# Kernel tuning notes

Hardware: AMD Instinct MI355X
Metric: run time of the kernel (lower is better)

The kernel has to match this reference:

```python
import jax, jax.numpy as jnp
import numpy as np

N = 1_048_576      # flattened batch (forward reshapes to (-1, 4))
Q_DIM = 4
HIDDEN = 64
DC = Q_DIM // 2    # q_dim_changed = 2
NUM_LO = (DC * DC - DC) // 2  # = 1
SLOPE = 0.01       # torch leaky_relu default negative slope


def setup_inputs() -> dict:
    key = jax.random.key(0)
    ks = jax.random.split(key, 9)
    def lin(kw, kb, fan_out, fan_in):
        bound = 1.0 / np.sqrt(fan_in)
        W = jax.random.uniform(kw, (fan_out, fan_in), jnp.float32, -bound, bound)
        b = jax.random.uniform(kb, (fan_out,), jnp.float32, -bound, bound)
        return W, b
    x = jax.random.normal(ks[0], (N, Q_DIM), jnp.float32)
    W1, b1 = lin(ks[1], ks[2], HIDDEN, Q_DIM)
    W2, b2 = lin(ks[3], ks[4], HIDDEN, HIDDEN)
    W_Ld, b_Ld = lin(ks[5], ks[6], DC, HIDDEN)
    W_Lo, b_Lo = lin(ks[7], ks[8], NUM_LO, HIDDEN)
    return {"x": x, "W1": W1, "b1": b1, "W2": W2, "b2": b2,
            "W_Ld": W_Ld, "b_Ld": b_Ld, "W_Lo": W_Lo, "b_Lo": b_Lo}


def reference(x, W1, b1, W2, b2, W_Ld, b_Ld, W_Lo, b_Lo):
    q = x.reshape(-1, Q_DIM)                      # (n, 4)
    n = q.shape[0]
    h1 = jax.nn.leaky_relu(q @ W1.T + b1, SLOPE)  # (n, 64)
    h2 = jax.nn.leaky_relu(h1 @ W2.T + b2, SLOPE) # (n, 64); dropout is eval-mode identity
    Ld = jax.nn.softplus(h2 @ W_Ld.T + b_Ld)      # (n, 2) positive diagonal
    Lo = h2 @ W_Lo.T + b_Lo                       # (n, 1) strictly-lower entries
    rows, cols = jnp.tril_indices(DC, -1)         # strictly lower triangle, row-major
    diag = jnp.arange(DC)
    L = jnp.zeros((n, DC, DC), dtype=q.dtype)
    L = L.at[:, rows, cols].set(Lo)               # scatter Lo (matches torch boolean-mask fill order)
    L = L.at[:, diag, diag].set(Ld)               # diag_embed(Ld)
    H = jnp.einsum('nij,nkj->nik', L, L) + 1e-9 * jnp.eye(DC, dtype=q.dtype)
    return H
```

## Files before the change

kernel.cpp:

```cpp
#include <hip/hip_runtime.h>


typedef __attribute__((ext_vector_type(8))) short bf16x8;
typedef __attribute__((ext_vector_type(4))) float f32x4;

#define ROWS_PER_BLOCK 256

__device__ __forceinline__ float lrelu(float a) {
    return fmaxf(a, 0.01f * a);
}

__device__ __forceinline__ float softplus(float v) {
    return fmaxf(v, 0.0f) + log1pf(expf(-fabsf(v)));
}

__device__ __forceinline__ unsigned cvt_pk_bf16(float lo, float hi) {
    unsigned r;
    asm("v_cvt_pk_bf16_f32 %0, %1, %2" : "=v"(r) : "v"(lo), "v"(hi));
    return r;
}

__global__ __launch_bounds__(256, 3) void dln_mfma(
    const float* __restrict__ x,
    const float* __restrict__ W1,  const float* __restrict__ b1,
    const float* __restrict__ W2,  const float* __restrict__ b2,
    const float* __restrict__ WLd, const float* __restrict__ bLd,
    const float* __restrict__ WLo, const float* __restrict__ bLo,
    float* __restrict__ out)
{
    __shared__ __align__(16) unsigned short h1s[4][8][64][8];

    const int tid  = threadIdx.x;
    const int lane = tid & 63;
    const int wv   = tid >> 6;
    const int quad = lane >> 4;
    const int c    = lane & 15;

    bf16x8 afrag[4][2];
    f32x4 wld0[4], wld1[4], wlo[4], b2v[4];
#pragma unroll
    for (int mt = 0; mt < 4; ++mt) {
        const float* wr = W2 + (16 * mt + c) * 64 + 8 * quad;
#pragma unroll
        for (int s = 0; s < 2; ++s) {
            const float4 f0 = *(const float4*)(wr + 32 * s);
            const float4 f1 = *(const float4*)(wr + 32 * s + 4);
            uint4 u;
            u.x = cvt_pk_bf16(f0.x, f0.y);
            u.y = cvt_pk_bf16(f0.z, f0.w);
            u.z = cvt_pk_bf16(f1.x, f1.y);
            u.w = cvt_pk_bf16(f1.z, f1.w);
            afrag[mt][s] = __builtin_bit_cast(bf16x8, u);
        }
        const int nb = 16 * mt + 4 * quad;
        wld0[mt] = *(const f32x4*)(WLd + nb);
        wld1[mt] = *(const f32x4*)(WLd + 64 + nb);
        wlo[mt]  = *(const f32x4*)(WLo + nb);
        b2v[mt]  = *(const f32x4*)(b2 + nb);
    }

    const int row_g = blockIdx.x * ROWS_PER_BLOCK + tid;
    {
        const float4 qv = ((const float4*)x)[row_g];
#pragma unroll
        for (int ch = 0; ch < 8; ++ch) {
            unsigned up[4];
#pragma unroll
            for (int p = 0; p < 4; ++p) {
                float h[2];
#pragma unroll
                for (int e = 0; e < 2; ++e) {
                    const int j = ch * 8 + p * 2 + e;
                    float a = b1[j];
                    a = fmaf(qv.x, W1[4 * j + 0], a);
                    a = fmaf(qv.y, W1[4 * j + 1], a);
                    a = fmaf(qv.z, W1[4 * j + 2], a);
                    a = fmaf(qv.w, W1[4 * j + 3], a);
                    h[e] = lrelu(a);
                }
                up[p] = cvt_pk_bf16(h[0], h[1]);
            }
            *(uint4*)&h1s[wv][ch][lane][0] = make_uint4(up[0], up[1], up[2], up[3]);
        }
    }

    float sld0 = 0.0f, sld1 = 0.0f, slo = 0.0f;
#pragma unroll
    for (int it = 0; it < 4; ++it) {
        const bf16x8 b0 = *(const bf16x8*)&h1s[wv][quad][it * 16 + c][0];
        const bf16x8 b1f = *(const bf16x8*)&h1s[wv][4 + quad][it * 16 + c][0];

        float pld0 = 0.0f, pld1 = 0.0f, plo = 0.0f;
#pragma unroll
        for (int mt = 0; mt < 4; ++mt) {
            f32x4 acc = b2v[mt];
            acc = __builtin_amdgcn_mfma_f32_16x16x32_bf16(afrag[mt][0], b0, acc, 0, 0, 0);
            acc = __builtin_amdgcn_mfma_f32_16x16x32_bf16(afrag[mt][1], b1f, acc, 0, 0, 0);
#pragma unroll
            for (int r = 0; r < 4; ++r) {
                const float h2 = lrelu(acc[r]);
                pld0 = fmaf(h2, wld0[mt][r], pld0);
                pld1 = fmaf(h2, wld1[mt][r], pld1);
                plo  = fmaf(h2, wlo[mt][r],  plo);
            }
        }
        pld0 += __shfl_xor(pld0, 16); pld0 += __shfl_xor(pld0, 32);
        pld1 += __shfl_xor(pld1, 16); pld1 += __shfl_xor(pld1, 32);
        plo  += __shfl_xor(plo,  16); plo  += __shfl_xor(plo,  32);
        if (it == quad) { sld0 = pld0; sld1 = pld1; slo = plo; }
    }

    {
        const float ld0 = softplus(sld0 + bLd[0]);
        const float ld1 = softplus(sld1 + bLd[1]);
        const float lo  = slo + bLo[0];
        float4 o;
        o.x = fmaf(ld0, ld0, 1e-9f);
        o.y = ld0 * lo;
        o.z = o.y;
        o.w = fmaf(lo, lo, fmaf(ld1, ld1, 1e-9f));
        reinterpret_cast<float4*>(out)[row_g] = o;
    }
}

__global__ __launch_bounds__(256) void dln_tail(
    const float* __restrict__ x,
    const float* __restrict__ W1,  const float* __restrict__ b1,
    const float* __restrict__ W2,  const float* __restrict__ b2,
    const float* __restrict__ WLd, const float* __restrict__ bLd,
    const float* __restrict__ WLo, const float* __restrict__ bLo,
    float* __restrict__ out, int row0, int nrows)
{
    const int row = row0 + blockIdx.x * 256 + threadIdx.x;
    if (row >= nrows) return;
    const float4 qv = reinterpret_cast<const float4*>(x)[row];
    float h1[64];
#pragma unroll
    for (int j = 0; j < 64; ++j) {
        float a = b1[j];
        a = fmaf(qv.x, W1[4 * j + 0], a);
        a = fmaf(qv.y, W1[4 * j + 1], a);
        a = fmaf(qv.z, W1[4 * j + 2], a);
        a = fmaf(qv.w, W1[4 * j + 3], a);
        h1[j] = lrelu(a);
    }
    float ld0 = bLd[0], ld1 = bLd[1], lo = bLo[0];
#pragma unroll 4
    for (int j = 0; j < 64; ++j) {
        float a0 = b2[j], a1 = 0.0f;
        const float* w = W2 + 64 * j;
#pragma unroll
        for (int k = 0; k < 64; k += 2) {
            a0 = fmaf(h1[k],     w[k],     a0);
            a1 = fmaf(h1[k + 1], w[k + 1], a1);
        }
        const float a = lrelu(a0 + a1);
        ld0 = fmaf(a, WLd[j],      ld0);
        ld1 = fmaf(a, WLd[64 + j], ld1);
        lo  = fmaf(a, WLo[j],      lo);
    }
    ld0 = softplus(ld0);
    ld1 = softplus(ld1);
    float4 o;
    o.x = fmaf(ld0, ld0, 1e-9f);
    o.y = ld0 * lo;
    o.z = o.y;
    o.w = fmaf(lo, lo, fmaf(ld1, ld1, 1e-9f));
    reinterpret_cast<float4*>(out)[row] = o;
}

extern "C" void kernel_launch(void* const* d_in, const int* in_sizes, int n_in,
                              void* d_out, int out_size, void* d_ws, size_t ws_size,
                              hipStream_t stream)
{
    const float* x   = (const float*)d_in[0];
    const float* W1  = (const float*)d_in[1];
    const float* b1  = (const float*)d_in[2];
    const float* W2  = (const float*)d_in[3];
    const float* b2  = (const float*)d_in[4];
    const float* WLd = (const float*)d_in[5];
    const float* bLd = (const float*)d_in[6];
    const float* WLo = (const float*)d_in[7];
    const float* bLo = (const float*)d_in[8];
    float* out = (float*)d_out;

    const int nrows = in_sizes[0] / 4;
    const int nfull = nrows / ROWS_PER_BLOCK;
    const int rem   = nrows - nfull * ROWS_PER_BLOCK;

    if (nfull > 0)
        dln_mfma<<<nfull, 256, 0, stream>>>(
            x, W1, b1, W2, b2, WLd, bLd, WLo, bLo, out);
    if (rem > 0)
        dln_tail<<<(rem + 255) / 256, 256, 0, stream>>>(
            x, W1, b1, W2, b2, WLd, bLd, WLo, bLo, out,
            nfull * ROWS_PER_BLOCK, nrows);
}
```

Measured before the change: 129.4 us.

## Process four 256-row groups per block to amortize weight fragment loads

Each block now handles 1024 rows by looping four times over 256-row groups. The W2 bf16 fragments and the head weights are loaded and converted once per block rather than once per 256 rows. All four x rows are prefetched up front, and the launch-bounds occupancy hint rises from 3 to 4. The trade-off is a quarter as many blocks, longer per-block serial work, and possibly more register pressure from the prefetched inputs. The intra-wave LDS reuse across iterations needs no barrier because each wave owns its own slice.

Result: slower. 164.1 us (+26.8%).

```diff
diff --git a/kernel.cpp b/kernel.cpp
--- a/kernel.cpp
+++ b/kernel.cpp
@@ -4,7 +4,8 @@
 typedef __attribute__((ext_vector_type(8))) short bf16x8;
 typedef __attribute__((ext_vector_type(4))) float f32x4;
 
-#define ROWS_PER_BLOCK 256
+#define ROWS_PER_BLOCK 1024
+#define G_ITERS 4
 
 __device__ __forceinline__ float lrelu(float a) {
     return fmaxf(a, 0.01f * a);
@@ -20,7 +21,7 @@
     return r;
 }
 
-__global__ __launch_bounds__(256, 3) void dln_mfma(
+__global__ __launch_bounds__(256, 4) void dln_mfma(
     const float* __restrict__ x,
     const float* __restrict__ W1,  const float* __restrict__ b1,
     const float* __restrict__ W2,  const float* __restrict__ b2,
@@ -35,6 +36,12 @@
     const int wv   = tid >> 6;
     const int quad = lane >> 4;
     const int c    = lane & 15;
+
+    const int row0 = blockIdx.x * ROWS_PER_BLOCK + tid;
+    const float4 qv0 = ((const float4*)x)[row0];
+    const float4 qv1 = ((const float4*)x)[row0 + 256];
+    const float4 qv2 = ((const float4*)x)[row0 + 512];
+    const float4 qv3 = ((const float4*)x)[row0 + 768];
 
     bf16x8 afrag[4][2];
     f32x4 wld0[4], wld1[4], wlo[4], b2v[4];
@@ -58,10 +65,15 @@
         wlo[mt]  = *(const f32x4*)(WLo + nb);
         b2v[mt]  = *(const f32x4*)(b2 + nb);
     }
-
-    const int row_g = blockIdx.x * ROWS_PER_BLOCK + tid;
-    {
-        const float4 qv = ((const float4*)x)[row_g];
+    const float bld0 = bLd[0];
+    const float bld1 = bLd[1];
+    const float blo0 = bLo[0];
+
+#pragma unroll
+    for (int g = 0; g < G_ITERS; ++g) {
+        const float4 qv = (g == 0) ? qv0 : (g == 1) ? qv1 : (g == 2) ? qv2 : qv3;
+        const int row_g = row0 + g * 256;
+
 #pragma unroll
         for (int ch = 0; ch < 8; ++ch) {
             unsigned up[4];
@@ -82,44 +94,44 @@
             }
             *(uint4*)&h1s[wv][ch][lane][0] = make_uint4(up[0], up[1], up[2], up[3]);
         }
-    }
-
-    float sld0 = 0.0f, sld1 = 0.0f, slo = 0.0f;
-#pragma unroll
-    for (int it = 0; it < 4; ++it) {
-        const bf16x8 b0 = *(const bf16x8*)&h1s[wv][quad][it * 16 + c][0];
-        const bf16x8 b1f = *(const bf16x8*)&h1s[wv][4 + quad][it * 16 + c][0];
-
-        float pld0 = 0.0f, pld1 = 0.0f, plo = 0.0f;
-#pragma unroll
-        for (int mt = 0; mt < 4; ++mt) {
-            f32x4 acc = b2v[mt];
-            acc = __builtin_amdgcn_mfma_f32_16x16x32_bf16(afrag[mt][0], b0, acc, 0, 0, 0);
-            acc = __builtin_amdgcn_mfma_f32_16x16x32_bf16(afrag[mt][1], b1f, acc, 0, 0, 0);
-#pragma unroll
-            for (int r = 0; r < 4; ++r) {
-                const float h2 = lrelu(acc[r]);
-                pld0 = fmaf(h2, wld0[mt][r], pld0);
-                pld1 = fmaf(h2, wld1[mt][r], pld1);
-                plo  = fmaf(h2, wlo[mt][r],  plo);
+
+        float sld0 = 0.0f, sld1 = 0.0f, slo = 0.0f;
+#pragma unroll
+        for (int it = 0; it < 4; ++it) {
+            const bf16x8 bf0 = *(const bf16x8*)&h1s[wv][quad][it * 16 + c][0];
+            const bf16x8 bf1 = *(const bf16x8*)&h1s[wv][4 + quad][it * 16 + c][0];
+
+            float pld0 = 0.0f, pld1 = 0.0f, plo = 0.0f;
+#pragma unroll
+            for (int mt = 0; mt < 4; ++mt) {
+                f32x4 acc = b2v[mt];
+                acc = __builtin_amdgcn_mfma_f32_16x16x32_bf16(afrag[mt][0], bf0, acc, 0, 0, 0);
+                acc = __builtin_amdgcn_mfma_f32_16x16x32_bf16(afrag[mt][1], bf1, acc, 0, 0, 0);
+#pragma unroll
+                for (int r = 0; r < 4; ++r) {
+                    const float h2 = lrelu(acc[r]);
+                    pld0 = fmaf(h2, wld0[mt][r], pld0);
+                    pld1 = fmaf(h2, wld1[mt][r], pld1);
+                    plo  = fmaf(h2, wlo[mt][r],  plo);
+                }
             }
-        }
-        pld0 += __shfl_xor(pld0, 16); pld0 += __shfl_xor(pld0, 32);
-        pld1 += __shfl_xor(pld1, 16); pld1 += __shfl_xor(pld1, 32);
-        plo  += __shfl_xor(plo,  16); plo  += __shfl_xor(plo,  32);
-        if (it == quad) { sld0 = pld0; sld1 = pld1; slo = plo; }
-    }
-
-    {
-        const float ld0 = softplus(sld0 + bLd[0]);
-        const float ld1 = softplus(sld1 + bLd[1]);
-        const float lo  = slo + bLo[0];
-        float4 o;
-        o.x = fmaf(ld0, ld0, 1e-9f);
-        o.y = ld0 * lo;
-        o.z = o.y;
-        o.w = fmaf(lo, lo, fmaf(ld1, ld1, 1e-9f));
-        reinterpret_cast<float4*>(out)[row_g] = o;
+            pld0 += __shfl_xor(pld0, 16); pld0 += __shfl_xor(pld0, 32);
+            pld1 += __shfl_xor(pld1, 16); pld1 += __shfl_xor(pld1, 32);
+            plo  += __shfl_xor(plo,  16); plo  += __shfl_xor(plo,  32);
+            if (it == quad) { sld0 = pld0; sld1 = pld1; slo = plo; }
+        }
+
+        {
+            const float ld0 = softplus(sld0 + bld0);
+            const float ld1 = softplus(sld1 + bld1);
+            const float lo  = slo + blo0;
+            float4 o;
+            o.x = fmaf(ld0, ld0, 1e-9f);
+            o.y = ld0 * lo;
+            o.z = o.y;
+            o.w = fmaf(lo, lo, fmaf(ld1, ld1, 1e-9f));
+            reinterpret_cast<float4*>(out)[row_g] = o;
+        }
     }
 }
 
```
